# Performance work log

Hardware: AMD Instinct MI355X
Metric: run time of the kernel (lower is better)

Reference implementation:

```python
import jax, jax.numpy as jnp
import numpy as np

B, S, E, H = 8, 512, 1024, 16
Dh = E // H
MAX_LEN = 512


def setup_inputs() -> dict:
    key = jax.random.key(0)
    ks = jax.random.split(key, 16)
    std = 1.0 / np.sqrt(E)
    inp = {
        "query": jax.random.normal(ks[0], (B, S, E), jnp.float32),
        "key": jax.random.normal(ks[1], (B, S, E), jnp.float32),
        "value": jax.random.normal(ks[2], (B, S, E), jnp.float32),
        "Wq": jax.random.normal(ks[3], (E, E), jnp.float32) * std,
        "bq": jax.random.normal(ks[4], (E,), jnp.float32) * std,
        "Wk": jax.random.normal(ks[5], (E, E), jnp.float32) * std,
        "bk": jax.random.normal(ks[6], (E,), jnp.float32) * std,
        "Wv": jax.random.normal(ks[7], (E, E), jnp.float32) * std,
        "bv": jax.random.normal(ks[8], (E,), jnp.float32) * std,
        "Wo": jax.random.normal(ks[9], (E, E), jnp.float32) * std,
        "bo": jax.random.normal(ks[10], (E,), jnp.float32) * std,
        "pos": jax.random.normal(ks[11], (MAX_LEN, 1, E), jnp.float32),
    }
    return inp


def reference(query, key, value, Wq, bq, Wk, bk, Wv, bv, Wo, bo, pos):
    b, sq, e = query.shape
    s = min(sq, key.shape[1])  # target_seq_length (static)
    scale = np.sqrt(Dh).astype(np.float32)
    pe = pos[:s, 0, :][None]  # [1, s, E] broadcast over batch
    q = query[:, :s] @ Wq.T + bq + pe
    k = key[:, :s] @ Wk.T + bk + pe
    v = value[:, :s] @ Wv.T + bv + pe
    # [b, s, H, Dh]
    q = q.reshape(b, s, H, Dh)
    k = k.reshape(b, s, H, Dh)
    v = v.reshape(b, s, H, Dh)
    scores = jnp.einsum("bqhd,bkhd->bhqk", q, k) / scale
    attn = jax.nn.softmax(scores, axis=-1)
    wv = jnp.einsum("bhqk,bkhd->bqhd", attn, v).reshape(b, s, e)
    return wv @ Wo.T + bo
```

## Files before the change

kernel.cpp:

```cpp
#include <hip/hip_runtime.h>
#include <hip/hip_bf16.h>

typedef __attribute__((ext_vector_type(8))) short bfx8;
typedef __attribute__((ext_vector_type(4))) short bfx4;
typedef __attribute__((ext_vector_type(4))) float fx4;

static __device__ __forceinline__ short f2bf(float f) {
  union { float f; unsigned u; } v; v.f = f;
  unsigned r = v.u + 0x7fffu + ((v.u >> 16) & 1u);
  return (short)(r >> 16);
}

static __device__ __forceinline__ void gld16(const void* g, void* l) {
  __builtin_amdgcn_global_load_lds(
      (const __attribute__((address_space(1))) void*)g,
      (__attribute__((address_space(3))) void*)l, 16, 0, 0);
}

constexpr int Bz = 8, Sq = 512, Em = 1024, Hn = 16, Dh = 64;
constexpr int Mrows = Bz * Sq;
constexpr size_t NE = (size_t)Mrows * Em;
constexpr size_t WE = (size_t)Em * Em;

__global__ __launch_bounds__(256) void convert_kernel(
    const float* __restrict__ q, const float* __restrict__ k,
    const float* __restrict__ v,
    const float* __restrict__ Wq, const float* __restrict__ Wk,
    const float* __restrict__ Wv, const float* __restrict__ Wo,
    short* __restrict__ qx, short* __restrict__ kx, short* __restrict__ vx,
    short* __restrict__ wqb, short* __restrict__ wkb,
    short* __restrict__ wvb, short* __restrict__ wob)
{
  const size_t c = (size_t)blockIdx.x * 256 + threadIdx.x;
  constexpr size_t CI = NE / 8;
  constexpr size_t CW = WE / 8;
  const float* src; short* dst; size_t off;
  if (c < 3 * CI) {
    const int sgi = (int)(c / CI);
    src = sgi == 0 ? q : sgi == 1 ? k : v;
    dst = sgi == 0 ? qx : sgi == 1 ? kx : vx;
    off = (c - (size_t)sgi * CI) * 8;
  } else {
    const size_t w = c - 3 * CI;
    const int sgi = (int)(w / CW);
    src = sgi == 0 ? Wq : sgi == 1 ? Wk : sgi == 2 ? Wv : Wo;
    dst = sgi == 0 ? wqb : sgi == 1 ? wkb : sgi == 2 ? wvb : wob;
    off = (w - (size_t)sgi * CW) * 8;
  }
  fx4 a = *(const fx4*)(src + off);
  fx4 b = *(const fx4*)(src + off + 4);
  bfx8 o = { f2bf(a[0]), f2bf(a[1]), f2bf(a[2]), f2bf(a[3]),
             f2bf(b[0]), f2bf(b[1]), f2bf(b[2]), f2bf(b[3]) };
  *(bfx8*)(dst + off) = o;
}

__global__ __launch_bounds__(512, 4) void gemm_qkv_bf16(
    const short* __restrict__ qx, const short* __restrict__ kx,
    const short* __restrict__ vx,
    const short* __restrict__ Wqb, const short* __restrict__ Wkb,
    const short* __restrict__ Wvb,
    const float* __restrict__ bq, const float* __restrict__ bk,
    const float* __restrict__ bv,
    const float* __restrict__ pos,
    short* __restrict__ qb, short* __restrict__ kb, short* __restrict__ vb)
{
  __shared__ short SM[24576];

  const int z = blockIdx.z;
  const short* X = (z == 0) ? qx : (z == 1) ? kx : vx;
  const short* W = (z == 0) ? Wqb : (z == 1) ? Wkb : Wvb;
  const float* bias = (z == 0) ? bq : (z == 1) ? bk : bv;
  short* dst = (z == 0) ? qb : (z == 1) ? kb : vb;

  const int t0b = blockIdx.x * 256;
  const int f0 = blockIdx.y * 128;
  const int t = threadIdx.x, lane = t & 63, wave = t >> 6;
  const int wf = wave & 1;
  const int wt = wave >> 1;
  const int fr = lane & 15, fq = lane >> 4;

  const int srow = t >> 2;
  const int scol = ((t & 3) ^ ((t >> 3) & 3)) * 8;
  const short* gA = W + (size_t)(f0 + srow) * Em + scol;
  const short* gB = X + (size_t)(t0b + srow) * Em + scol;
  const int ldst = wave * 512;

  auto stage = [&](int ktn, int s) {
    short* base = SM + s * 12288;
    const int ko = ktn * 32;
    gld16(gA + ko, base + ldst);
    gld16(gB + ko, base + 4096 + ldst);
    gld16(gB + (size_t)128 * Em + ko, base + 8192 + ldst);
  };

  const int csw = (fq ^ ((fr >> 1) & 3)) * 8;

  fx4 acc[4][4] = {};

  stage(0, 0);
  __builtin_amdgcn_sched_barrier(0);
  asm volatile("s_waitcnt vmcnt(0)");
  __builtin_amdgcn_sched_barrier(0);
  __builtin_amdgcn_s_barrier();

  for (int kt = 0; kt < 32; ++kt) {
    const int s = kt & 1;
    const short* bA = SM + s * 12288;
    const short* bB = bA + 4096;
    const bool pre = (kt + 1 < 32);
    if (pre) stage(kt + 1, s ^ 1);
    __builtin_amdgcn_sched_barrier(0);

    bfx8 af[4], bf[4];
#pragma unroll
    for (int u = 0; u < 4; ++u)
      af[u] = *(const bfx8*)&bA[(wf * 64 + u * 16 + fr) * 32 + csw];
#pragma unroll
    for (int v = 0; v < 4; ++v)
      bf[v] = *(const bfx8*)&bB[(wt * 64 + v * 16 + fr) * 32 + csw];

    __builtin_amdgcn_s_setprio(1);
#pragma unroll
    for (int u = 0; u < 4; ++u)
#pragma unroll
      for (int v = 0; v < 4; ++v)
        acc[u][v] = __builtin_amdgcn_mfma_f32_16x16x32_bf16(af[u], bf[v], acc[u][v], 0, 0, 0);
    __builtin_amdgcn_s_setprio(0);
    __builtin_amdgcn_sched_barrier(0);

    if (pre) asm volatile("s_waitcnt vmcnt(0)");
    __builtin_amdgcn_sched_barrier(0);
    __builtin_amdgcn_s_barrier();
  }

  const int b = t0b >> 9;
  if (z < 2) {
#pragma unroll
    for (int p = 0; p < 2; ++p) {
      if (p) __syncthreads();
      if ((wt >> 1) == p) {
#pragma unroll
        for (int u = 0; u < 4; ++u) {
          const int nloc = wf * 64 + u * 16 + fq * 4;
          const int nng = f0 + nloc;
          const fx4 bb = *(const fx4*)&bias[nng];
#pragma unroll
          for (int v = 0; v < 4; ++v) {
            const int token = wt * 64 + v * 16 + fr;
            const int tl = token - p * 128;
            const int s = (t0b + token) & (Sq - 1);
            const fx4 pe = *(const fx4*)&pos[(size_t)s * Em + nng];
            const fx4 a = acc[u][v];
            bfx4 o = { f2bf(a[0] + bb[0] + pe[0]), f2bf(a[1] + bb[1] + pe[1]),
                       f2bf(a[2] + bb[2] + pe[2]), f2bf(a[3] + bb[3] + pe[3]) };
            *(bfx4*)&SM[tl * 136 + nloc] = o;
          }
        }
      }
      __syncthreads();
#pragma unroll
      for (int it = 0; it < 4; ++it) {
        const int flat = it * 512 + t;
        const int tl = flat >> 4, ch = flat & 15;
        bfx8 val = *(const bfx8*)&SM[tl * 136 + ch * 8];
        const int nng = f0 + ch * 8;
        const int h = nng >> 6, d = nng & 63;
        const int s = (t0b + p * 128 + tl) & (Sq - 1);
        *(bfx8*)&dst[(((size_t)b * Hn + h) * Sq + s) * Dh + d] = val;
      }
    }
  } else {
#pragma unroll
    for (int fp = 0; fp < 2; ++fp) {
      if (fp) __syncthreads();
      if (wf == fp) {
#pragma unroll
        for (int u = 0; u < 4; ++u) {
          const int nloc = u * 16 + fq * 4;
          const int nng = f0 + fp * 64 + nloc;
          const fx4 bb = *(const fx4*)&bias[nng];
#pragma unroll
          for (int v = 0; v < 4; ++v) {
            const int token = wt * 64 + v * 16 + fr;
            const int s = (t0b + token) & (Sq - 1);
            const fx4 pe = *(const fx4*)&pos[(size_t)s * Em + nng];
            const fx4 a = acc[u][v];
#pragma unroll
            for (int i = 0; i < 4; ++i) {
              const int row = nloc + i;
              SM[row * 264 + (token ^ ((row & 12) << 2))] = f2bf(a[i] + bb[i] + pe[i]);
            }
          }
        }
      }
      __syncthreads();
      const int s0 = t0b & (Sq - 1);
#pragma unroll
      for (int it = 0; it < 4; ++it) {
        const int flat = it * 512 + t;
        const int row = flat >> 5, ch = flat & 31;
        bfx8 val = *(const bfx8*)&SM[row * 264 + ((ch * 8) ^ ((row & 12) << 2))];
        const int nng = f0 + fp * 64 + row;
        const int h = nng >> 6, d = nng & 63;
        *(bfx8*)&dst[(((size_t)b * Hn + h) * Dh + d) * Sq + s0 + ch * 8] = val;
      }
    }
  }
}

__global__ __launch_bounds__(256, 4) void gemm_out_bf16(
    const short* __restrict__ wv, const short* __restrict__ Wob,
    const float* __restrict__ bo, float* __restrict__ out)
{
  __shared__ short As[128 * 64];
  __shared__ short Bs[64 * 64];

  const int m0 = blockIdx.x * 64;
  const int n0 = blockIdx.y * 128;
  const int t = threadIdx.x, lane = t & 63, wave = t >> 6;
  const int wr = wave >> 1, wc = wave & 1;
  const int fr = lane & 15, fq = lane >> 4;

  const int trow = t >> 3;
  const int scol = ((t & 7) ^ (trow & 7)) * 8;
  const short* gW = Wob + (size_t)(n0 + trow) * Em + scol;
  const short* gX = wv + (size_t)(m0 + trow) * Em + scol;
  const int lofs = wave * 512;

  const int sw0 = ((fq ^ (fr & 7)) * 8);
  const int sw1 = (((4 + fq) ^ (fr & 7)) * 8);

  fx4 acc[4][2] = {};

  for (int k0 = 0; k0 < Em; k0 += 64) {
#pragma unroll
    for (int g = 0; g < 4; ++g)
      gld16(gW + (size_t)(32 * g) * Em + k0, As + g * 2048 + lofs);
#pragma unroll
    for (int g = 0; g < 2; ++g)
      gld16(gX + (size_t)(32 * g) * Em + k0, Bs + g * 2048 + lofs);
    __syncthreads();

#pragma unroll
    for (int ks = 0; ks < 2; ++ks) {
      const int sw = ks ? sw1 : sw0;
      bfx8 af[4], bf[2];
#pragma unroll
      for (int u = 0; u < 4; ++u)
        af[u] = *(const bfx8*)&As[(wr * 64 + u * 16 + fr) * 64 + sw];
#pragma unroll
      for (int v = 0; v < 2; ++v)
        bf[v] = *(const bfx8*)&Bs[(wc * 32 + v * 16 + fr) * 64 + sw];
#pragma unroll
      for (int u = 0; u < 4; ++u)
#pragma unroll
        for (int v = 0; v < 2; ++v)
          acc[u][v] = __builtin_amdgcn_mfma_f32_16x16x32_bf16(af[u], bf[v], acc[u][v], 0, 0, 0);
    }
    __syncthreads();
  }

#pragma unroll
  for (int u = 0; u < 4; ++u) {
    const int nn = n0 + wr * 64 + u * 16 + fq * 4;
    const fx4 bb = *(const fx4*)&bo[nn];
#pragma unroll
    for (int v = 0; v < 2; ++v) {
      const int m = m0 + wc * 32 + v * 16 + fr;
      fx4 val = acc[u][v];
      val[0] += bb[0]; val[1] += bb[1]; val[2] += bb[2]; val[3] += bb[3];
      *(fx4*)&out[(size_t)m * Em + nn] = val;
    }
  }
}

constexpr int KVB = 64, LDK = 72;

__global__ __launch_bounds__(512) void attn_kernel(
    const short* __restrict__ qb, const short* __restrict__ kb,
    const short* __restrict__ vb, short* __restrict__ wv)
{
  __shared__ short Ks[KVB * LDK];
  __shared__ short Vt[Dh * LDK];
  __shared__ short Ps[8][16 * LDK];

  const int bh = blockIdx.x;
  const int qt = blockIdx.y;
  const int t = threadIdx.x, lane = t & 63, wave = t >> 6;
  const int fr = lane & 15, fq = lane >> 4;

  const size_t base = (size_t)bh * Sq * Dh;
  const int q0 = qt * 128 + wave * 16;

  bfx8 qf[2];
  {
    const short* qp = qb + base + (size_t)(q0 + fr) * Dh;
    qf[0] = *(const bfx8*)(qp + fq * 8);
    qf[1] = *(const bfx8*)(qp + 32 + fq * 8);
  }

  const int kr = t >> 3, kc = (t & 7) * 8;
  const short* kbp = kb + base + (size_t)kr * Dh + kc;
  const short* vbp = vb + base + (size_t)kr * Sq + kc;

  {
    bfx8 k0 = *(const bfx8*)kbp;
    bfx8 v0 = *(const bfx8*)vbp;
    *(bfx8*)&Ks[kr * LDK + kc] = k0;
    *(bfx8*)&Vt[kr * LDK + kc] = v0;
  }
  __syncthreads();

  float mrow[4] = { -1e30f, -1e30f, -1e30f, -1e30f };
  float lrow[4] = { 0.f, 0.f, 0.f, 0.f };
  fx4 oacc[4] = {};

  for (int kv0 = 0; kv0 < Sq; kv0 += KVB) {
    const bool more = (kv0 + KVB) < Sq;
    bfx8 nk0, nv0;
    if (more) {
      nk0 = *(const bfx8*)(kbp + (size_t)(kv0 + KVB) * Dh);
      nv0 = *(const bfx8*)(vbp + kv0 + KVB);
    }

    fx4 sa[4] = {};
    __builtin_amdgcn_s_setprio(1);
#pragma unroll
    for (int nf = 0; nf < 4; ++nf) {
#pragma unroll
      for (int ks = 0; ks < 2; ++ks) {
        bfx8 kf = *(const bfx8*)&Ks[(nf * 16 + fr) * LDK + ks * 32 + fq * 8];
        sa[nf] = __builtin_amdgcn_mfma_f32_16x16x32_bf16(qf[ks], kf, sa[nf], 0, 0, 0);
      }
    }
    __builtin_amdgcn_s_setprio(0);

#pragma unroll
    for (int i = 0; i < 4; ++i) {
      float mx = fmaxf(fmaxf(sa[0][i], sa[1][i]), fmaxf(sa[2][i], sa[3][i]));
      mx = fmaxf(mx, __shfl_xor(mx, 1));
      mx = fmaxf(mx, __shfl_xor(mx, 2));
      mx = fmaxf(mx, __shfl_xor(mx, 4));
      mx = fmaxf(mx, __shfl_xor(mx, 8));
      mx *= 0.125f;
      if (mx > mrow[i] + 8.f) {
        const float alpha = __expf(mrow[i] - mx);
        mrow[i] = mx;
        lrow[i] *= alpha;
#pragma unroll
        for (int df = 0; df < 4; ++df) oacc[df][i] *= alpha;
      }
      float rs = 0.f;
#pragma unroll
      for (int nf = 0; nf < 4; ++nf) {
        const float p = __expf(sa[nf][i] * 0.125f - mrow[i]);
        rs += p;
        Ps[wave][(fq * 4 + i) * LDK + nf * 16 + fr] = f2bf(p);
      }
      rs += __shfl_xor(rs, 1);
      rs += __shfl_xor(rs, 2);
      rs += __shfl_xor(rs, 4);
      rs += __shfl_xor(rs, 8);
      lrow[i] += rs;
    }

    bfx8 pf[2];
    pf[0] = *(const bfx8*)&Ps[wave][fr * LDK + fq * 8];
    pf[1] = *(const bfx8*)&Ps[wave][fr * LDK + 32 + fq * 8];
    __builtin_amdgcn_s_setprio(1);
#pragma unroll
    for (int df = 0; df < 4; ++df) {
#pragma unroll
      for (int ks = 0; ks < 2; ++ks) {
        bfx8 vf = *(const bfx8*)&Vt[(df * 16 + fr) * LDK + ks * 32 + fq * 8];
        oacc[df] = __builtin_amdgcn_mfma_f32_16x16x32_bf16(pf[ks], vf, oacc[df], 0, 0, 0);
      }
    }
    __builtin_amdgcn_s_setprio(0);
    __syncthreads();

    if (more) {
      *(bfx8*)&Ks[kr * LDK + kc] = nk0;
      *(bfx8*)&Vt[kr * LDK + kc] = nv0;
      __syncthreads();
    }
  }

  const int b = bh >> 4, h = bh & 15;
#pragma unroll
  for (int df = 0; df < 4; ++df) {
    const int d = df * 16 + fr;
#pragma unroll
    for (int i = 0; i < 4; ++i) {
      const int qrow = q0 + fq * 4 + i;
      const float o = oacc[df][i] / lrow[i];
      wv[((size_t)b * Sq + qrow) * Em + h * Dh + d] = f2bf(o);
    }
  }
}

extern "C" void kernel_launch(void* const* d_in, const int* in_sizes, int n_in,
                              void* d_out, int out_size, void* d_ws, size_t ws_size,
                              hipStream_t stream) {
  (void)in_sizes; (void)n_in; (void)out_size; (void)ws_size;
  const float* query = (const float*)d_in[0];
  const float* key   = (const float*)d_in[1];
  const float* value = (const float*)d_in[2];
  const float* Wq = (const float*)d_in[3];
  const float* bq = (const float*)d_in[4];
  const float* Wk = (const float*)d_in[5];
  const float* bk = (const float*)d_in[6];
  const float* Wv = (const float*)d_in[7];
  const float* bv = (const float*)d_in[8];
  const float* Wo = (const float*)d_in[9];
  const float* bo = (const float*)d_in[10];
  const float* pos = (const float*)d_in[11];

  short* qx = (short*)d_ws;
  short* kx = qx + NE;
  short* vx = kx + NE;
  short* Wqb = vx + NE;
  short* Wkb = Wqb + WE;
  short* Wvb = Wkb + WE;
  short* Wob = Wvb + WE;
  short* qb = Wob + WE;
  short* wv = qx;
  short* kb = (short*)d_out;
  short* vb = kb + NE;

  convert_kernel<<<dim3(8192), 256, 0, stream>>>(
      query, key, value, Wq, Wk, Wv, Wo, qx, kx, vx, Wqb, Wkb, Wvb, Wob);
  gemm_qkv_bf16<<<dim3(Mrows / 256, Em / 128, 3), 512, 0, stream>>>(
      qx, kx, vx, Wqb, Wkb, Wvb, bq, bk, bv, pos, qb, kb, vb);
  attn_kernel<<<dim3(Bz * Hn, Sq / 128), 512, 0, stream>>>(qb, kb, vb, wv);
  gemm_out_bf16<<<dim3(Mrows / 64, Em / 128), 256, 0, stream>>>(
      wv, Wob, bo, (float*)d_out);
}
```

Before: 103.5 us.

## Fuse fp32-to-bf16 activation conversion into QKV GEMM operand staging

The separate conversion pass over query/key/value is removed. The QKV GEMM now loads fp32 activations into registers one k-step ahead, converts them to bf16, and writes them into swizzled LDS after the MFMA block, while the weight tile still uses direct global-to-LDS loads. This cuts a full write and re-read of three activation tensors in bf16. The cost is more register pressure and VALU conversion work inside the GEMM loop, and the fp32 reads fetch twice the bytes per tile, with the same values re-read by each of the eight column blocks.

```diff
diff --git a/kernel.cpp b/kernel.cpp
--- a/kernel.cpp
+++ b/kernel.cpp
@@ -23,30 +23,17 @@
 constexpr size_t WE = (size_t)Em * Em;
 
 __global__ __launch_bounds__(256) void convert_kernel(
-    const float* __restrict__ q, const float* __restrict__ k,
-    const float* __restrict__ v,
     const float* __restrict__ Wq, const float* __restrict__ Wk,
     const float* __restrict__ Wv, const float* __restrict__ Wo,
-    short* __restrict__ qx, short* __restrict__ kx, short* __restrict__ vx,
     short* __restrict__ wqb, short* __restrict__ wkb,
     short* __restrict__ wvb, short* __restrict__ wob)
 {
   const size_t c = (size_t)blockIdx.x * 256 + threadIdx.x;
-  constexpr size_t CI = NE / 8;
   constexpr size_t CW = WE / 8;
-  const float* src; short* dst; size_t off;
-  if (c < 3 * CI) {
-    const int sgi = (int)(c / CI);
-    src = sgi == 0 ? q : sgi == 1 ? k : v;
-    dst = sgi == 0 ? qx : sgi == 1 ? kx : vx;
-    off = (c - (size_t)sgi * CI) * 8;
-  } else {
-    const size_t w = c - 3 * CI;
-    const int sgi = (int)(w / CW);
-    src = sgi == 0 ? Wq : sgi == 1 ? Wk : sgi == 2 ? Wv : Wo;
-    dst = sgi == 0 ? wqb : sgi == 1 ? wkb : sgi == 2 ? wvb : wob;
-    off = (w - (size_t)sgi * CW) * 8;
-  }
+  const int sgi = (int)(c / CW);
+  const float* src = sgi == 0 ? Wq : sgi == 1 ? Wk : sgi == 2 ? Wv : Wo;
+  short* dst = sgi == 0 ? wqb : sgi == 1 ? wkb : sgi == 2 ? wvb : wob;
+  const size_t off = (c - (size_t)sgi * CW) * 8;
   fx4 a = *(const fx4*)(src + off);
   fx4 b = *(const fx4*)(src + off + 4);
   bfx8 o = { f2bf(a[0]), f2bf(a[1]), f2bf(a[2]), f2bf(a[3]),
@@ -55,8 +42,8 @@
 }
 
 __global__ __launch_bounds__(512, 4) void gemm_qkv_bf16(
-    const short* __restrict__ qx, const short* __restrict__ kx,
-    const short* __restrict__ vx,
+    const float* __restrict__ qf, const float* __restrict__ kf,
+    const float* __restrict__ vf,
     const short* __restrict__ Wqb, const short* __restrict__ Wkb,
     const short* __restrict__ Wvb,
     const float* __restrict__ bq, const float* __restrict__ bk,
@@ -67,7 +54,7 @@
   __shared__ short SM[24576];
 
   const int z = blockIdx.z;
-  const short* X = (z == 0) ? qx : (z == 1) ? kx : vx;
+  const float* Xf = (z == 0) ? qf : (z == 1) ? kf : vf;
   const short* W = (z == 0) ? Wqb : (z == 1) ? Wkb : Wvb;
   const float* bias = (z == 0) ? bq : (z == 1) ? bk : bv;
   short* dst = (z == 0) ? qb : (z == 1) ? kb : vb;
@@ -80,37 +67,50 @@
   const int fr = lane & 15, fq = lane >> 4;
 
   const int srow = t >> 2;
-  const int scol = ((t & 3) ^ ((t >> 3) & 3)) * 8;
-  const short* gA = W + (size_t)(f0 + srow) * Em + scol;
-  const short* gB = X + (size_t)(t0b + srow) * Em + scol;
+  const int sccA = ((t & 3) ^ ((t >> 3) & 3)) * 8;
+  const short* gA = W + (size_t)(f0 + srow) * Em + sccA;
   const int ldst = wave * 512;
 
-  auto stage = [&](int ktn, int s) {
-    short* base = SM + s * 12288;
-    const int ko = ktn * 32;
-    gld16(gA + ko, base + ldst);
-    gld16(gB + ko, base + 4096 + ldst);
-    gld16(gB + (size_t)128 * Em + ko, base + 8192 + ldst);
+  const int rB = t >> 1, cp = t & 1;
+  const float* gBf = Xf + (size_t)(t0b + rB) * Em + cp * 16;
+  const int swrB = (rB >> 1) & 3;
+  const int pB0 = ((cp * 2) ^ swrB) * 8;
+  const int pB1 = ((cp * 2 + 1) ^ swrB) * 8;
+
+  const int csw = (fq ^ ((fr >> 1) & 3)) * 8;
+
+  fx4 acc[4][4] = {};
+  fx4 r0, r1, r2, r3;
+
+  auto stageA = [&](int ktn, int s) { gld16(gA + ktn * 32, SM + s * 12288 + ldst); };
+  auto loadB = [&](int ktn) {
+    const float* p = gBf + ktn * 32;
+    r0 = *(const fx4*)p; r1 = *(const fx4*)(p + 4);
+    r2 = *(const fx4*)(p + 8); r3 = *(const fx4*)(p + 12);
   };
-
-  const int csw = (fq ^ ((fr >> 1) & 3)) * 8;
-
-  fx4 acc[4][4] = {};
-
-  stage(0, 0);
-  __builtin_amdgcn_sched_barrier(0);
-  asm volatile("s_waitcnt vmcnt(0)");
-  __builtin_amdgcn_sched_barrier(0);
-  __builtin_amdgcn_s_barrier();
+  auto writeB = [&](int s) {
+    short* base = SM + s * 12288 + 4096 + rB * 32;
+    bfx8 lo = { f2bf(r0[0]), f2bf(r0[1]), f2bf(r0[2]), f2bf(r0[3]),
+                f2bf(r1[0]), f2bf(r1[1]), f2bf(r1[2]), f2bf(r1[3]) };
+    bfx8 hi = { f2bf(r2[0]), f2bf(r2[1]), f2bf(r2[2]), f2bf(r2[3]),
+                f2bf(r3[0]), f2bf(r3[1]), f2bf(r3[2]), f2bf(r3[3]) };
+    *(bfx8*)&base[pB0] = lo;
+    *(bfx8*)&base[pB1] = hi;
+  };
+
+  stageA(0, 0);
+  loadB(0);
+  writeB(0);
+  __syncthreads();
 
   for (int kt = 0; kt < 32; ++kt) {
     const int s = kt & 1;
+    const bool pre = (kt + 1 < 32);
+    if (pre) { stageA(kt + 1, s ^ 1); loadB(kt + 1); }
+    __builtin_amdgcn_sched_barrier(0);
+
     const short* bA = SM + s * 12288;
     const short* bB = bA + 4096;
-    const bool pre = (kt + 1 < 32);
-    if (pre) stage(kt + 1, s ^ 1);
-    __builtin_amdgcn_sched_barrier(0);
-
     bfx8 af[4], bf[4];
 #pragma unroll
     for (int u = 0; u < 4; ++u)
@@ -128,9 +128,8 @@
     __builtin_amdgcn_s_setprio(0);
     __builtin_amdgcn_sched_barrier(0);
 
-    if (pre) asm volatile("s_waitcnt vmcnt(0)");
-    __builtin_amdgcn_sched_barrier(0);
-    __builtin_amdgcn_s_barrier();
+    if (pre) writeB(s ^ 1);
+    __syncthreads();
   }
 
   const int b = t0b >> 9;
@@ -416,22 +415,19 @@
   const float* bo = (const float*)d_in[10];
   const float* pos = (const float*)d_in[11];
 
-  short* qx = (short*)d_ws;
-  short* kx = qx + NE;
-  short* vx = kx + NE;
-  short* Wqb = vx + NE;
+  short* Wqb = (short*)d_ws;
   short* Wkb = Wqb + WE;
   short* Wvb = Wkb + WE;
   short* Wob = Wvb + WE;
   short* qb = Wob + WE;
-  short* wv = qx;
+  short* wv = qb + NE;
   short* kb = (short*)d_out;
   short* vb = kb + NE;
 
-  convert_kernel<<<dim3(8192), 256, 0, stream>>>(
-      query, key, value, Wq, Wk, Wv, Wo, qx, kx, vx, Wqb, Wkb, Wvb, Wob);
+  convert_kernel<<<dim3(2048), 256, 0, stream>>>(
+      Wq, Wk, Wv, Wo, Wqb, Wkb, Wvb, Wob);
   gemm_qkv_bf16<<<dim3(Mrows / 256, Em / 128, 3), 512, 0, stream>>>(
-      qx, kx, vx, Wqb, Wkb, Wvb, bq, bk, bv, pos, qb, kb, vb);
+      query, key, value, Wqb, Wkb, Wvb, bq, bk, bv, pos, qb, kb, vb);
   attn_kernel<<<dim3(Bz * Hn, Sq / 128), 512, 0, stream>>>(qb, kb, vb, wv);
   gemm_out_bf16<<<dim3(Mrows / 64, Em / 128), 256, 0, stream>>>(
       wv, Wob, bo, (float*)d_out);
```

Result: slower. 108.7 us (+5.0%).
